# Kernel tuning notes

Hardware: AMD Instinct MI355X
Metric: run time of the kernel (lower is better)

The kernel has to match this reference:

```python
import jax, jax.numpy as jnp
import numpy as np

B, S, E = 2, 2048, 1024
H = 1344            # hidden_dim = ceil(1.3*1024/64)*64
NH = 4              # mLSTM heads
DH = H // NH        # 336
K = 4               # causal conv kernel size
NPH = H // 4        # headwise proj heads (qkv_proj_blocksize=4)
PD = H // NPH       # per-head proj dim = 4
EPS = 1e-6


def setup_inputs() -> dict:
    key = jax.random.key(0)
    ks = jax.random.split(key, 10)
    s_in = jnp.sqrt(2.0 / (5 * E))    # small_init(E)
    s_pd = jnp.sqrt(2.0 / (5 * PD))   # small_init per-head dim
    return {
        "x": jax.random.normal(ks[0], (B, S, E), jnp.float32),
        "W_up": jax.random.normal(ks[1], (E, 2 * H), jnp.float32) * s_in,
        "conv_k": jax.random.normal(ks[2], (K, 1, H), jnp.float32) * jnp.sqrt(2.0 / K),  # depthwise, WIO layout
        "conv_b": jnp.zeros((H,), jnp.float32),
        "Wq": jax.random.normal(ks[3], (NPH, PD, PD), jnp.float32) * s_pd,
        "Wk": jax.random.normal(ks[4], (NPH, PD, PD), jnp.float32) * s_pd,
        "Wv": jax.random.normal(ks[5], (NPH, PD, PD), jnp.float32) * s_pd,
        "W_ig": jax.random.normal(ks[6], (3 * H, NH), jnp.float32) * 0.01,
        "b_ig": jax.random.normal(ks[7], (NH,), jnp.float32) * 0.1,
        "W_fg": jax.random.normal(ks[8], (3 * H, NH), jnp.float32) * 0.01,
        "b_fg": jnp.linspace(3.0, 6.0, NH, dtype=jnp.float32),
        "ln_w": jnp.ones((H,), jnp.float32),
        "skip": jnp.ones((H,), jnp.float32),
        "W_down": jax.random.normal(ks[9], (H, E), jnp.float32) * (2.0 / 12 / np.sqrt(H)),
    }


def _headwise(x, W):
    # LinearHeadwiseExpand: block-diagonal projection over NPH heads of size PD
    xh = x.reshape(B, S, NPH, PD)
    return jnp.einsum('bshd,hdo->bsho', xh, W).reshape(B, S, H)


def _mlstm_cell(q, k, v, ig, fg):
    # parallel stabilized mLSTM; q,k,v: (B,NH,S,DH); ig,fg: (B,NH,S)
    logf = jax.nn.log_sigmoid(fg)
    c = jnp.cumsum(logf, axis=-1)                         # (B,NH,S)
    logfmat = c[..., :, None] - c[..., None, :]           # (B,NH,S,S) cumulative forget decay
    mask = jnp.tril(jnp.ones((S, S), bool))               # causal mask
    log_D = jnp.where(mask, logfmat, -jnp.inf) + ig[..., None, :]
    m = jnp.max(log_D, axis=-1, keepdims=True)            # rowwise stabilizer
    D = jnp.exp(log_D - m)
    qk = jnp.einsum('bnsd,bntd->bnst', q, k) * (DH ** -0.5)
    C = qk * D
    n = jnp.maximum(jnp.abs(jnp.sum(C, axis=-1, keepdims=True)), jnp.exp(-m))
    return jnp.einsum('bnst,bntd->bnsd', C / (n + EPS), v)


def reference(x, W_up, conv_k, conv_b, Wq, Wk, Wv, W_ig, b_ig, W_fg, b_fg, ln_w, skip, W_down):
    x_inner = x @ W_up                                    # (B,S,2H)
    x_m, z = jnp.split(x_inner, 2, axis=-1)
    # depthwise causal conv1d
    xp = jnp.pad(x_m, ((0, 0), (K - 1, 0), (0, 0)))
    xc = jax.lax.conv_general_dilated(
        xp, conv_k, (1,), 'VALID',
        dimension_numbers=('NWC', 'WIO', 'NWC'),
        feature_group_count=H) + conv_b
    act = jax.nn.silu(xc)
    q = _headwise(act, Wq)
    k = _headwise(act, Wk)
    v = _headwise(x_m, Wv)
    gin = jnp.concatenate([q, k, v], axis=-1)             # (B,S,3H)
    ig = jnp.transpose(gin @ W_ig + b_ig, (0, 2, 1))      # (B,NH,S)
    fg = jnp.transpose(gin @ W_fg + b_fg, (0, 2, 1))
    qh = jnp.transpose(q.reshape(B, S, NH, DH), (0, 2, 1, 3))
    kh = jnp.transpose(k.reshape(B, S, NH, DH), (0, 2, 1, 3))
    vh = jnp.transpose(v.reshape(B, S, NH, DH), (0, 2, 1, 3))
    h = _mlstm_cell(qh, kh, vh, ig, fg)                   # (B,NH,S,DH)
    # multi-head layernorm (per-head groupnorm over DH, scale only)
    mu = jnp.mean(h, axis=-1, keepdims=True)
    var = jnp.var(h, axis=-1, keepdims=True)
    hn = (h - mu) * jax.lax.rsqrt(var + 1e-5) * ln_w.reshape(NH, 1, DH)
    h_out = jnp.transpose(hn, (0, 2, 1, 3)).reshape(B, S, H)
    h_state = (h_out + skip * act) * jax.nn.silu(z)
    return h_state @ W_down
```

## Files before the change

### kernel.cpp

```cpp
#include <hip/hip_runtime.h>
#include <cmath>

#define DI __device__ __forceinline__

constexpr int B_=2, S_=2048, E_=1024, H_=1344, NH_=4, DH_=336;
constexpr int BS_=B_*S_, H2_=2*H_;
constexpr int NG_=B_*NH_*S_;

constexpr size_t N_X=(size_t)BS_*E_;
constexpr size_t N_WUP=(size_t)E_*H2_;
constexpr size_t N_WDN=(size_t)H_*E_;
constexpr size_t N_BSH=(size_t)BS_*H_;
constexpr size_t N_BSH2=(size_t)BS_*H2_;
constexpr size_t N_WH=5376, N_WG=16128, N_CK=4*H_;

constexpr size_t O_IGB = 64;
constexpr size_t O_LOGF= O_IGB + NG_;
constexpr size_t O_AB  = O_LOGF+ NG_;
constexpr size_t O_MB  = O_AB  + NG_;
constexpr size_t O_MTB = O_MB  + NG_;
constexpr size_t O_CK  = O_MTB + NG_;
constexpr size_t O_CB  = O_CK  + N_CK;
constexpr size_t O_WQ  = O_CB  + H_;
constexpr size_t O_WK  = O_WQ  + N_WH;
constexpr size_t O_WV  = O_WK  + N_WH;
constexpr size_t O_WIG = O_WV  + N_WH;
constexpr size_t O_BIG = O_WIG + N_WG;
constexpr size_t O_WFG = O_BIG + 16;
constexpr size_t O_BFG = O_WFG + N_WG;
constexpr size_t O_LNW = O_BFG + 16;
constexpr size_t O_SKP = O_LNW + H_;
constexpr size_t O_FX  = O_SKP + H_;
constexpr size_t O_FWUP= O_FX  + N_X;
constexpr size_t O_FWDN= O_FWUP+ N_WUP;
constexpr size_t O_XIN = O_FWDN+ N_WDN;
constexpr size_t O_ACT = O_XIN + N_BSH2;
constexpr size_t O_QB  = O_ACT + N_BSH;
constexpr size_t O_KB  = O_QB  + N_BSH;
constexpr size_t O_VB  = O_KB  + N_BSH;
constexpr size_t O_HOUT= O_VB  + N_BSH;

constexpr size_t KSPLIT_SHORTS=(size_t)8*128*11*64*8;
constexpr size_t VT_SHORTS=(size_t)8*64*22*64*8;

typedef __attribute__((ext_vector_type(8))) short bf16x8;
typedef __attribute__((ext_vector_type(4))) float f32x4;

DI float bf2f(unsigned int u){union{unsigned int i;float f;}v;v.i=(u&0xffffu)<<16;return v.f;}
DI unsigned short f2bf(float f){union{float f;unsigned int i;}v;v.f=f;unsigned int x=v.i;
  return (unsigned short)((x+0x7fffu+((x>>16)&1u))>>16);}
DI float siluf(float x){return x/(1.f+expf(-x));}
DI float logsigf(float x){return (x>=0.f)?-log1pf(expf(-x)):x-log1pf(expf(x));}
DI void load4(const float* p, float* d){float4 v=*reinterpret_cast<const float4*>(p);
  d[0]=v.x;d[1]=v.y;d[2]=v.z;d[3]=v.w;}

__global__ __launch_bounds__(256) void detect_k(const unsigned short* __restrict__ xraw,
                                                int* __restrict__ flag){
  __shared__ int cnt_s;
  if(threadIdx.x==0) cnt_s=0;
  __syncthreads();
  int c=0;
  for(int i=threadIdx.x;i<2048;i+=256){
    const unsigned e=(xraw[i]>>7)&0xFFu;
    if(e>=0x90u) c++;
  }
  atomicAdd(&cnt_s,c);
  __syncthreads();
  if(threadIdx.x==0) *flag=(cnt_s>16)?0:1;
}

constexpr int CV0=5376, CV1=CV0+1344, CV2=CV1+5376, CV3=CV2+5376, CV4=CV3+5376,
              CV5=CV4+16128, CV6=CV5+4, CV7=CV6+16128, CV8=CV7+4,
              CV9=CV8+1344, CVT=CV9+1344;
__global__ __launch_bounds__(256) void convall_k(
    const void* s0,const void* s1,const void* s2,const void* s3,const void* s4,
    const void* s5,const void* s6,const void* s7,const void* s8,const void* s9,
    const void* s10, float* __restrict__ ws, const int* __restrict__ flag){
  const int i=blockIdx.x*256+threadIdx.x;
  if(i>=CVT) return;
  const void* src; int off; size_t dst;
  if(i<CV0){src=s0; off=i;      dst=O_CK +off;}
  else if(i<CV1){src=s1; off=i-CV0; dst=O_CB +off;}
  else if(i<CV2){src=s2; off=i-CV1; dst=O_WQ +off;}
  else if(i<CV3){src=s3; off=i-CV2; dst=O_WK +off;}
  else if(i<CV4){src=s4; off=i-CV3; dst=O_WV +off;}
  else if(i<CV5){src=s5; off=i-CV4; dst=O_WIG+off;}
  else if(i<CV6){src=s6; off=i-CV5; dst=O_BIG+off;}
  else if(i<CV7){src=s7; off=i-CV6; dst=O_WFG+off;}
  else if(i<CV8){src=s8; off=i-CV7; dst=O_BFG+off;}
  else if(i<CV9){src=s9; off=i-CV8; dst=O_LNW+off;}
  else          {src=s10;off=i-CV9; dst=O_SKP+off;}
  ws[dst]=(*flag)?bf2f(((const unsigned short*)src)[off])
                 :((const float*)src)[off];
}

__global__ __launch_bounds__(256) void aprep_k(const void* __restrict__ src,
                                               const int* __restrict__ flag,
                                               int kcn,int ldk,int total,
                                               unsigned short* __restrict__ hi,
                                               unsigned short* __restrict__ lo){
  const int slot=blockIdx.x*256+threadIdx.x;
  if(slot>=total) return;
  const int l=slot&63, rest=slot>>6;
  const int kc=rest%kcn, mt=rest/kcn;
  const int row=mt*16+(l&15), k0=kc*32+(l>>4)*8;
  const int fl=flag?*flag:0;
  float v[8];
  if(fl){
    const unsigned short* s=(const unsigned short*)src+(size_t)row*ldk+k0;
    const uint4 u=*reinterpret_cast<const uint4*>(s);
    v[0]=bf2f(u.x);v[1]=bf2f(u.x>>16);v[2]=bf2f(u.y);v[3]=bf2f(u.y>>16);
    v[4]=bf2f(u.z);v[5]=bf2f(u.z>>16);v[6]=bf2f(u.w);v[7]=bf2f(u.w>>16);
  }else{
    const float* s=(const float*)src+(size_t)row*ldk+k0;
    load4(s,v); load4(s+4,v+4);
  }
  unsigned short h8[8], l8[8];
#pragma unroll
  for(int j=0;j<8;j++){ h8[j]=f2bf(v[j]); l8[j]=f2bf(v[j]-bf2f(h8[j])); }
  uint4 ph,pl;
  ph.x=(unsigned)h8[0]|((unsigned)h8[1]<<16); ph.y=(unsigned)h8[2]|((unsigned)h8[3]<<16);
  ph.z=(unsigned)h8[4]|((unsigned)h8[5]<<16); ph.w=(unsigned)h8[6]|((unsigned)h8[7]<<16);
  pl.x=(unsigned)l8[0]|((unsigned)l8[1]<<16); pl.y=(unsigned)l8[2]|((unsigned)l8[3]<<16);
  pl.z=(unsigned)l8[4]|((unsigned)l8[5]<<16); pl.w=(unsigned)l8[6]|((unsigned)l8[7]<<16);
  *reinterpret_cast<uint4*>(&hi[(size_t)slot*8])=ph;
  *reinterpret_cast<uint4*>(&lo[(size_t)slot*8])=pl;
}

__global__ __launch_bounds__(256) void bprep_k(const void* __restrict__ src,
                                               const int* __restrict__ flag,
                                               int kcn,int ldn,int total,
                                               unsigned short* __restrict__ hi,
                                               unsigned short* __restrict__ lo){
  const int slot=blockIdx.x*256+threadIdx.x;
  if(slot>=total) return;
  const int l=slot&63, rest=slot>>6;
  const int kc=rest%kcn, nt=rest/kcn;
  const int col=nt*16+(l&15), row0=kc*32+(l>>4)*8;
  const int fl=flag?*flag:0;
  float v[8];
  if(fl){
    const unsigned short* s=(const unsigned short*)src;
#pragma unroll
    for(int j=0;j<8;j++) v[j]=bf2f(s[(size_t)(row0+j)*ldn+col]);
  }else{
    const float* s=(const float*)src;
#pragma unroll
    for(int j=0;j<8;j++) v[j]=s[(size_t)(row0+j)*ldn+col];
  }
  unsigned short h8[8], l8[8];
#pragma unroll
  for(int j=0;j<8;j++){ h8[j]=f2bf(v[j]); l8[j]=f2bf(v[j]-bf2f(h8[j])); }
  uint4 ph,pl;
  ph.x=(unsigned)h8[0]|((unsigned)h8[1]<<16); ph.y=(unsigned)h8[2]|((unsigned)h8[3]<<16);
  ph.z=(unsigned)h8[4]|((unsigned)h8[5]<<16); ph.w=(unsigned)h8[6]|((unsigned)h8[7]<<16);
  pl.x=(unsigned)l8[0]|((unsigned)l8[1]<<16); pl.y=(unsigned)l8[2]|((unsigned)l8[3]<<16);
  pl.z=(unsigned)l8[4]|((unsigned)l8[5]<<16); pl.w=(unsigned)l8[6]|((unsigned)l8[7]<<16);
  *reinterpret_cast<uint4*>(&hi[(size_t)slot*8])=ph;
  *reinterpret_cast<uint4*>(&lo[(size_t)slot*8])=pl;
}

__global__ __launch_bounds__(256) void gemm2_k(
    const unsigned short* __restrict__ Ahi, const unsigned short* __restrict__ Alo,
    const unsigned short* __restrict__ Bhi, const unsigned short* __restrict__ Blo,
    void* __restrict__ C, const int* __restrict__ flag, int kcn, int ldc){
  const int t=threadIdx.x, w=t>>6, l=t&63, lm=l&15, quad=l>>4;
  const int bn=blockIdx.x*128, bm=blockIdx.y*128;
  const int mtg0=bm>>4, ntg0=bn>>4;

  __shared__ short TT[2][32*512];

  f32x4 acc[2][8];
#pragma unroll
  for(int g=0;g<2;g++)
#pragma unroll
    for(int nt=0;nt<8;nt++) acc[g][nt]={0.f,0.f,0.f,0.f};

  auto stage=[&](int buf,int kc){
#pragma unroll
    for(int j=0;j<8;j++){
      const int tr=w*8+j;
      const unsigned short* src;
      if(tr<8)       src=&Ahi[((size_t)(mtg0+tr   )*kcn+kc)*512+(size_t)l*8];
      else if(tr<16) src=&Alo[((size_t)(mtg0+tr-8 )*kcn+kc)*512+(size_t)l*8];
      else if(tr<24) src=&Bhi[((size_t)(ntg0+tr-16)*kcn+kc)*512+(size_t)l*8];
      else           src=&Blo[((size_t)(ntg0+tr-24)*kcn+kc)*512+(size_t)l*8];
      __builtin_amdgcn_global_load_lds(
        (const __attribute__((address_space(1))) unsigned int*)src,
        (__attribute__((address_space(3))) unsigned int*)&TT[buf][tr*512],
        16,0,0);
    }
  };

  auto compute=[&](int buf){
    const short* Tb=&TT[buf][0];
    const bf16x8 ah0=*reinterpret_cast<const bf16x8*>(&Tb[(2*w  )*512+l*8]);
    const bf16x8 ah1=*reinterpret_cast<const bf16x8*>(&Tb[(2*w+1)*512+l*8]);
    const bf16x8 al0=*reinterpret_cast<const bf16x8*>(&Tb[(8+2*w  )*512+l*8]);
    const bf16x8 al1=*reinterpret_cast<const bf16x8*>(&Tb[(8+2*w+1)*512+l*8]);
#pragma unroll
    for(int nt=0;nt<8;nt++){
      const bf16x8 bh=*reinterpret_cast<const bf16x8*>(&Tb[(16+nt)*512+l*8]);
      const bf16x8 bl=*reinterpret_cast<const bf16x8*>(&Tb[(24+nt)*512+l*8]);
      acc[0][nt]=__builtin_amdgcn_mfma_f32_16x16x32_bf16(ah0,bh,acc[0][nt],0,0,0);
      acc[0][nt]=__builtin_amdgcn_mfma_f32_16x16x32_bf16(al0,bh,acc[0][nt],0,0,0);
      acc[0][nt]=__builtin_amdgcn_mfma_f32_16x16x32_bf16(ah0,bl,acc[0][nt],0,0,0);
      acc[1][nt]=__builtin_amdgcn_mfma_f32_16x16x32_bf16(ah1,bh,acc[1][nt],0,0,0);
      acc[1][nt]=__builtin_amdgcn_mfma_f32_16x16x32_bf16(al1,bh,acc[1][nt],0,0,0);
      acc[1][nt]=__builtin_amdgcn_mfma_f32_16x16x32_bf16(ah1,bl,acc[1][nt],0,0,0);
    }
  };

  stage(0,0);
  __syncthreads();
  for(int kc=0;kc<kcn;kc++){
    const int cur=kc&1;
    if(kc+1<kcn) stage(cur^1,kc+1);
    compute(cur);
    __syncthreads();
  }

  const int bf=flag?*flag:0;
#pragma unroll
  for(int g=0;g<2;g++)
#pragma unroll
    for(int nt=0;nt<8;nt++)
#pragma unroll
      for(int r=0;r<4;r++){
        const size_t idx=(size_t)(bm+(2*w+g)*16+quad*4+r)*ldc+bn+nt*16+lm;
        if(bf) ((unsigned short*)C)[idx]=f2bf(acc[g][nt][r]);
        else   ((float*)C)[idx]=acc[g][nt][r];
      }
}

__global__ __launch_bounds__(256) void convqkv_k(const float* __restrict__ xin,
                                                 const float* __restrict__ ck,
                                                 const float* __restrict__ cb,
                                                 const float* __restrict__ Wq,
                                                 const float* __restrict__ Wk,
                                                 const float* __restrict__ Wv,
                                                 float* __restrict__ act,
                                                 float* __restrict__ qb,
                                                 float* __restrict__ kb,
                                                 float* __restrict__ vb){
  const int i=blockIdx.x*256+threadIdx.x;
  if(i>=BS_*(H_/4)) return;
  const int bs=i/(H_/4), ph=i-bs*(H_/4);
  const int b=bs>>11, s=bs&2047;
  const int base=ph*4;
  float xc[4];
#pragma unroll
  for(int d=0;d<4;d++) xc[d]=cb[base+d];
  float xm[4]={0.f,0.f,0.f,0.f};
#pragma unroll
  for(int w=0;w<4;w++){
    const int sr=s-3+w;
    if(sr>=0){
      float xv[4];
      load4(&xin[(size_t)(b*S_+sr)*H2_+base],xv);
#pragma unroll
      for(int d=0;d<4;d++) xc[d]+=xv[d]*ck[w*H_+base+d];
      if(w==3){ xm[0]=xv[0];xm[1]=xv[1];xm[2]=xv[2];xm[3]=xv[3]; }
    }
  }
  float a4[4];
#pragma unroll
  for(int d=0;d<4;d++) a4[d]=siluf(xc[d]);
  *reinterpret_cast<float4*>(&act[(size_t)bs*H_+base])
      =make_float4(a4[0],a4[1],a4[2],a4[3]);
  float q4[4],k4[4],v4[4];
#pragma unroll
  for(int o=0;o<4;o++){
    float q=0.f,k=0.f,v=0.f;
#pragma unroll
    for(int d=0;d<4;d++){
      q+=a4[d]*Wq[ph*16+d*4+o];
      k+=a4[d]*Wk[ph*16+d*4+o];
      v+=xm[d]*Wv[ph*16+d*4+o];
    }
    q4[o]=q;k4[o]=k;v4[o]=v;
  }
  const int nh=ph/84, dh0=(ph-nh*84)*4;
  const size_t off=((size_t)(b*NH_+nh)*S_+s)*DH_+dh0;
  *reinterpret_cast<float4*>(&qb[off])=make_float4(q4[0],q4[1],q4[2],q4[3]);
  *reinterpret_cast<float4*>(&kb[off])=make_float4(k4[0],k4[1],k4[2],k4[3]);
  *reinterpret_cast<float4*>(&vb[off])=make_float4(v4[0],v4[1],v4[2],v4[3]);
}

__global__ __launch_bounds__(256) void gates2_k(const float* __restrict__ qb,
                                                const float* __restrict__ kb,
                                                const float* __restrict__ vb,
                                                const float* __restrict__ Wig,
                                                const float* __restrict__ big,
                                                const float* __restrict__ Wfg,
                                                const float* __restrict__ bfg,
                                                float* __restrict__ igb,
                                                float* __restrict__ logfb){
  const int wid=(blockIdx.x*256+threadIdx.x)>>6;
  const int l=threadIdx.x&63;
  if(wid>=BS_) return;
  const int b=wid>>11, s=wid&2047;
  float aI0=0.f,aI1=0.f,aI2=0.f,aI3=0.f;
  float aF0=0.f,aF1=0.f,aF2=0.f,aF3=0.f;
  for(int nh=0;nh<NH_;nh++){
    const size_t rb=((size_t)(b*NH_+nh)*S_+s)*DH_;
    const int hb=nh*DH_;
    for(int dh=l;dh<DH_;dh+=64){
      const int h=hb+dh;
      const float q=qb[rb+dh], k=kb[rb+dh], v=vb[rb+dh];
      const float4 wiq=*reinterpret_cast<const float4*>(&Wig[(size_t)h*4]);
      const float4 wik=*reinterpret_cast<const float4*>(&Wig[(size_t)(H_+h)*4]);
      const float4 wiv=*reinterpret_cast<const float4*>(&Wig[(size_t)(2*H_+h)*4]);
      const float4 wfq=*reinterpret_cast<const float4*>(&Wfg[(size_t)h*4]);
      const float4 wfk=*reinterpret_cast<const float4*>(&Wfg[(size_t)(H_+h)*4]);
      const float4 wfv=*reinterpret_cast<const float4*>(&Wfg[(size_t)(2*H_+h)*4]);
      aI0+=q*wiq.x+k*wik.x+v*wiv.x;
      aI1+=q*wiq.y+k*wik.y+v*wiv.y;
      aI2+=q*wiq.z+k*wik.z+v*wiv.z;
      aI3+=q*wiq.w+k*wik.w+v*wiv.w;
      aF0+=q*wfq.x+k*wfk.x+v*wfv.x;
      aF1+=q*wfq.y+k*wfk.y+v*wfv.y;
      aF2+=q*wfq.z+k*wfk.z+v*wfv.z;
      aF3+=q*wfq.w+k*wfk.w+v*wfv.w;
    }
  }
#pragma unroll
  for(int m=1;m<64;m<<=1){
    aI0+=__shfl_xor(aI0,m); aI1+=__shfl_xor(aI1,m);
    aI2+=__shfl_xor(aI2,m); aI3+=__shfl_xor(aI3,m);
    aF0+=__shfl_xor(aF0,m); aF1+=__shfl_xor(aF1,m);
    aF2+=__shfl_xor(aF2,m); aF3+=__shfl_xor(aF3,m);
  }
  if(l==0){
    const size_t o0=(size_t)(b*NH_+0)*S_+s;
    const size_t o1=(size_t)(b*NH_+1)*S_+s;
    const size_t o2=(size_t)(b*NH_+2)*S_+s;
    const size_t o3=(size_t)(b*NH_+3)*S_+s;
    igb[o0]=aI0+big[0]; igb[o1]=aI1+big[1];
    igb[o2]=aI2+big[2]; igb[o3]=aI3+big[3];
    logfb[o0]=logsigf(aF0+bfg[0]); logfb[o1]=logsigf(aF1+bfg[1]);
    logfb[o2]=logsigf(aF2+bfg[2]); logfb[o3]=logsigf(aF3+bfg[3]);
  }
}

__global__ __launch_bounds__(256) void kprep_k(const float* __restrict__ kb,
                                               unsigned short* __restrict__ khi,
                                               unsigned short* __restrict__ klo){
  const int blk=blockIdx.x;
  const int head=blk>>7, tt=blk&127;
  const size_t obase=(size_t)blk*11*512;
  for(int slot=threadIdx.x; slot<704; slot+=256){
    const int dc=slot>>6, ll=slot&63, quad=ll>>4, lm=ll&15;
    const int tg=tt*16+lm, dbase=dc*32+quad*8;
    float v[8];
    if(dbase<336){
      load4(&kb[((size_t)head*S_+tg)*DH_+dbase],v);
      load4(&kb[((size_t)head*S_+tg)*DH_+dbase+4],v+4);
    } else { for(int j=0;j<8;j++) v[j]=0.f; }
    unsigned short hi8[8], lo8[8];
#pragma unroll
    for(int j=0;j<8;j++){
      hi8[j]=f2bf(v[j]);
      lo8[j]=f2bf(v[j]-bf2f(hi8[j]));
    }
    const size_t o=obase+(size_t)(dc*64+ll)*8;
    uint4 ph, pl;
    ph.x=(unsigned)hi8[0]|((unsigned)hi8[1]<<16); ph.y=(unsigned)hi8[2]|((unsigned)hi8[3]<<16);
    ph.z=(unsigned)hi8[4]|((unsigned)hi8[5]<<16); ph.w=(unsigned)hi8[6]|((unsigned)hi8[7]<<16);
    pl.x=(unsigned)lo8[0]|((unsigned)lo8[1]<<16); pl.y=(unsigned)lo8[2]|((unsigned)lo8[3]<<16);
    pl.z=(unsigned)lo8[4]|((unsigned)lo8[5]<<16); pl.w=(unsigned)lo8[6]|((unsigned)lo8[7]<<16);
    *reinterpret_cast<uint4*>(&khi[o])=ph;
    *reinterpret_cast<uint4*>(&klo[o])=pl;
  }
}

__global__ __launch_bounds__(256) void vprep_k(const float* __restrict__ vb,
                                               unsigned short* __restrict__ vTf){
  const int blk=blockIdx.x;
  const int head=blk>>6, tc=blk&63;
  const size_t obase=(size_t)blk*22*512;
  for(int slot=threadIdx.x; slot<1408; slot+=256){
    const int ntg=slot>>6, ll=slot&63, quad=ll>>4, lm=ll&15;
    const int n=ntg*16+lm, t0=tc*32+quad*8;
    unsigned short h8[8];
#pragma unroll
    for(int j=0;j<8;j++){
      float val;
      if(n<336)       val=vb[((size_t)head*S_+t0+j)*DH_+n];
      else if(n==336) val=1.f;
      else            val=0.f;
      h8[j]=f2bf(val);
    }
    uint4 pk;
    pk.x=(unsigned)h8[0]|((unsigned)h8[1]<<16); pk.y=(unsigned)h8[2]|((unsigned)h8[3]<<16);
    pk.z=(unsigned)h8[4]|((unsigned)h8[5]<<16); pk.w=(unsigned)h8[6]|((unsigned)h8[7]<<16);
    *reinterpret_cast<uint4*>(&vTf[obase+(size_t)(ntg*64+ll)*8])=pk;
  }
}

__global__ __launch_bounds__(256) void scan_k(const float* __restrict__ igb,
                                              const float* __restrict__ logfb,
                                              float* __restrict__ ab,float* __restrict__ Mb,
                                              float* __restrict__ mtb){
  const int head=blockIdx.x, t=threadIdx.x;
  __shared__ float sh[256];
  const float* lf=logfb+(size_t)head*S_;
  const float* ig=igb+(size_t)head*S_;
  float lc[8];
  float run=0.f;
#pragma unroll
  for(int i=0;i<8;i++){ run+=lf[t*8+i]; lc[i]=run; }
  sh[t]=run;
  for(int st=1;st<256;st<<=1){
    __syncthreads();
    const float v=(t>=st)?sh[t-st]:0.f;
    __syncthreads();
    sh[t]+=v;
  }
  __syncthreads();
  const float off=(t==0)?0.f:sh[t-1];
  __syncthreads();
  float av[8],mv[8],cv[8];
  float mrun=-1e30f;
#pragma unroll
  for(int i=0;i<8;i++){
    cv[i]=off+lc[i];
    av[i]=ig[t*8+i]-cv[i];
    mrun=fmaxf(mrun,av[i]);
    mv[i]=mrun;
  }
  sh[t]=mrun;
  for(int st=1;st<256;st<<=1){
    __syncthreads();
    const float v=(t>=st)?sh[t-st]:-1e30f;
    __syncthreads();
    sh[t]=fmaxf(sh[t],v);
  }
  __syncthreads();
  const float moff=(t==0)?-1e30f:sh[t-1];
#pragma unroll
  for(int i=0;i<8;i++){
    const float Mi=fmaxf(moff,mv[i]);
    const size_t j=(size_t)head*S_+t*8+i;
    ab[j]=av[i]; Mb[j]=Mi; mtb[j]=cv[i]+Mi;
  }
}

__global__ __launch_bounds__(512,1) void mlstm6_k(
    const float* __restrict__ qb, const unsigned short* __restrict__ khi,
    const unsigned short* __restrict__ klo, const unsigned short* __restrict__ vTf,
    const float* __restrict__ ab, const float* __restrict__ Mb,
    float* __restrict__ part, float* __restrict__ rsum){
  const int bid=blockIdx.x;
  const int head=bid&7;
  const int rest=bid>>3;
  const int pairI=rest&7, seg=rest>>3;
  const int t=threadIdx.x, w=t>>6, l=t&63, lm=l&15, quad=l>>4;

  __shared__ short KV[2][66*512];
  __shared__ short Sc[8][16][40];

  const size_t hb=(size_t)head*S_;
  const float scale=0.05455447256f;

  const int sbA=pairI, sbB=15-pairI;
  const int nA=pairI+1, nTot=17;

  bf16x8 qh[11], ql[11];
  f32x4 accO[22];
  float Mr[4];
  int ws0=sbA*128+w*16;

  auto loadQ=[&](int ws0_){
    const float* qrow=qb+(hb+ws0_+lm)*DH_;
#pragma unroll
    for(int dc=0;dc<11;dc++){
      const int dbase=dc*32+quad*8;
      float v[8];
      if(dbase<336){ load4(qrow+dbase,v); load4(qrow+dbase+4,v+4); }
      else { for(int j=0;j<8;j++) v[j]=0.f; }
#pragma unroll
      for(int j=0;j<8;j++){
        const unsigned short h=f2bf(v[j]);
        qh[dc][j]=(short)h;
        ql[dc][j]=(short)f2bf(v[j]-bf2f(h));
      }
    }
#pragma unroll
    for(int r=0;r<4;r++) Mr[r]=Mb[hb+ws0_+quad*4+r];
#pragma unroll
    for(int n=0;n<22;n++) accO[n]={0.f,0.f,0.f,0.f};
  };

  auto itemC=[&](int i)->int{
    return (i<nA)? (seg+4*i) : (seg+4*(i-nA));
  };

  auto stage=[&](int buf,int c){
    const size_t kbase=(((size_t)head*128+(size_t)(2*c))*11)*512+(size_t)l*8;
    const size_t vbase=(((size_t)head*64+(size_t)c)*22)*512+(size_t)l*8;
#pragma unroll
    for(int j=0;j<9;j++){
      const int tr=w+8*j;
      if(tr<66){
        const unsigned short* src;
        if(tr<22)      src=&khi[kbase+(size_t)tr*512];
        else if(tr<44) src=&klo[kbase+(size_t)(tr-22)*512];
        else           src=&vTf[vbase+(size_t)(tr-44)*512];
        __builtin_amdgcn_global_load_lds(
          (const __attribute__((address_space(1))) unsigned int*)src,
          (__attribute__((address_space(3))) unsigned int*)&KV[buf][(size_t)tr*512],
          16,0,0);
      }
    }
  };

  auto compute=[&](int c,int buf){
    const int t0=c<<5;
    if(t0>ws0+15) return;
    const float al0=ab[hb+t0+lm];
    const float al1=ab[hb+t0+16+lm];
#pragma unroll
    for(int tt=0;tt<2;tt++){
      f32x4 a0={0,0,0,0}, a1={0,0,0,0}, a2={0,0,0,0};
#pragma unroll
      for(int dc=0;dc<11;dc++){
        const bf16x8 kh=*reinterpret_cast<const bf16x8*>(&KV[buf][(tt*11+dc)*512+l*8]);
        const bf16x8 kl=*reinterpret_cast<const bf16x8*>(&KV[buf][(22+tt*11+dc)*512+l*8]);
        a0=__builtin_amdgcn_mfma_f32_16x16x32_bf16(qh[dc],kh,a0,0,0,0);
        a1=__builtin_amdgcn_mfma_f32_16x16x32_bf16(ql[dc],kh,a1,0,0,0);
        a2=__builtin_amdgcn_mfma_f32_16x16x32_bf16(qh[dc],kl,a2,0,0,0);
      }
      const float al=(tt==0)?al0:al1;
      const int tg=t0+tt*16+lm;
#pragma unroll
      for(int r=0;r<4;r++){
        const int srow=quad*4+r;
        const float qk=a0[r]+a1[r]+a2[r];
        const float e=fminf(al-Mr[r],0.f);
        const float msk=(tg<=ws0+srow)?1.f:0.f;
        Sc[w][srow][tt*16+lm]=(short)f2bf(msk*(qk*scale*expf(e)));
      }
    }
    const bf16x8 scf=*reinterpret_cast<const bf16x8*>(&Sc[w][lm][quad*8]);
#pragma unroll
    for(int nt=0;nt<22;nt++){
      const bf16x8 vf=*reinterpret_cast<const bf16x8*>(&KV[buf][(44+nt)*512+l*8]);
      accO[nt]=__builtin_amdgcn_mfma_f32_16x16x32_bf16(scf,vf,accO[nt],0,0,0);
    }
  };

  auto epilogue=[&](){
    const size_t pbase=(size_t)head*2048+ws0;
#pragma unroll
    for(int nt=0;nt<22;nt++){
      const int col=nt*16+lm;
#pragma unroll
      for(int r=0;r<4;r++){
        const int srow=quad*4+r;
        const float val=accO[nt][r];
        if(col<336){ if(val!=0.f) atomicAdd(&part[(pbase+srow)*336+col],val); }
        else if(col==336){ if(val!=0.f) atomicAdd(&rsum[pbase+srow],val); }
      }
    }
  };

  loadQ(ws0);
  stage(0,itemC(0));
  __syncthreads();
  int cur=0;
  for(int i=0;i<nTot;i++){
    if(i+1<nTot) stage(cur^1,itemC(i+1));
    compute(itemC(i),cur);
    if(i==nA-1){
      epilogue();
      ws0=sbB*128+w*16;
      loadQ(ws0);
    }
    __syncthreads();
    cur^=1;
  }
  epilogue();
}

__global__ __launch_bounds__(256) void finalize2_k(const float* __restrict__ part,
                                                   const float* __restrict__ rsum,
                                                   const float* __restrict__ mtb,
                                                   const float* __restrict__ lnw,
                                                   const float* __restrict__ skip,
                                                   const float* __restrict__ act,
                                                   const float* __restrict__ xin,
                                                   float* __restrict__ hs){
  const int sblk=blockIdx.x, head=blockIdx.y;
  const int bI=head>>2, nh=head&3;
  const int s0=sblk*32;
  const int t=threadIdx.x, row=t>>3, sub=t&7;
  __shared__ float red1[32][8], red2[32][8];
  __shared__ float mu_s[32], rs_s[32], inv_s[32];
  const size_t pbase=(size_t)head*2048+s0;
  const float* prow=part+(pbase+row)*336;
  float s1=0.f,s2=0.f;
  for(int c=sub;c<336;c+=8){ const float v=prow[c]; s1+=v; s2+=v*v; }
  red1[row][sub]=s1; red2[row][sub]=s2;
  __syncthreads();
  if(sub==0){
    float a1=0.f,a2=0.f;
#pragma unroll
    for(int j=0;j<8;j++){ a1+=red1[row][j]; a2+=red2[row][j]; }
    const float mt=mtb[(size_t)head*S_+s0+row];
    const float nn=fmaxf(fabsf(rsum[pbase+row]), expf(fminf(fmaxf(-mt,-60.f),60.f)));
    const float inv=1.f/(nn+1e-6f);
    const float mu=a1*inv/336.f;
    const float var=a2*inv*inv/336.f-mu*mu;
    inv_s[row]=inv; mu_s[row]=mu;
    rs_s[row]=rsqrtf(fmaxf(var,0.f)+1e-5f);
  }
  __syncthreads();
  const float inv=inv_s[row], mu=mu_s[row], rs=rs_s[row];
  const size_t bsrow=(size_t)(bI*S_+s0+row);
  float* orow=hs+bsrow*H_+nh*DH_;
  const float* arow=act+bsrow*H_+nh*DH_;
  const float* zrow=xin+bsrow*H2_+H_+nh*DH_;
  const float* srw=skip+nh*DH_;
  const float* lrw=lnw+nh*DH_;
  for(int c=sub;c<336;c+=8){
    const float hn=(prow[c]*inv-mu)*rs*lrw[c];
    orow[c]=(hn+srw[c]*arow[c])*siluf(zrow[c]);
  }
}

extern "C" void kernel_launch(void* const* d_in, const int* in_sizes, int n_in,
                              void* d_out, int out_size, void* d_ws, size_t ws_size,
                              hipStream_t stream){
  float* ws=(float*)d_ws;
  int* flag=(int*)ws;

  float* igb  = ws+O_IGB;
  float* logfb= ws+O_LOGF;
  float* ab   = ws+O_AB;
  float* Mbuf = ws+O_MB;
  float* mtb  = ws+O_MTB;
  float* f_ck = ws+O_CK;
  float* f_cb = ws+O_CB;
  float* f_wq = ws+O_WQ;
  float* f_wk = ws+O_WK;
  float* f_wv = ws+O_WV;
  float* f_wig= ws+O_WIG;
  float* f_big= ws+O_BIG;
  float* f_wfg= ws+O_WFG;
  float* f_bfg= ws+O_BFG;
  float* f_lnw= ws+O_LNW;
  float* f_skp= ws+O_SKP;
  float* xin  = ws+O_XIN;
  float* act  = ws+O_ACT;
  float* qb   = ws+O_QB;
  float* kb   = ws+O_KB;
  float* vb   = ws+O_VB;

  unsigned short* xhi  =(unsigned short*)(ws+O_FX);   unsigned short* xlo  =xhi+N_X;
  unsigned short* wuphi=(unsigned short*)(ws+O_FWUP); unsigned short* wuplo=wuphi+N_WUP;
  unsigned short* wdnhi=(unsigned short*)(ws+O_FWDN); unsigned short* wdnlo=wdnhi+N_WDN;
  unsigned short* khi=(unsigned short*)(ws+O_FX);
  unsigned short* klo=khi+KSPLIT_SHORTS;
  unsigned short* vTf=(unsigned short*)kb;
  unsigned short* hshi=(unsigned short*)kb;
  unsigned short* hslo=hshi+N_BSH;
  float* partb=vb;
  float* rsumb=igb;
  float* hs   = qb;

  detect_k<<<1,256,0,stream>>>((const unsigned short*)d_in[0],flag);
  convall_k<<<(CVT+255)/256,256,0,stream>>>(d_in[2],d_in[3],d_in[4],d_in[5],d_in[6],
                                            d_in[7],d_in[8],d_in[9],d_in[10],d_in[11],
                                            d_in[12],ws,flag);

  aprep_k<<<(256*32*64+255)/256,256,0,stream>>>(d_in[0],flag,32,1024,256*32*64,xhi,xlo);
  bprep_k<<<(168*32*64+255)/256,256,0,stream>>>(d_in[1],flag,32,2688,168*32*64,wuphi,wuplo);
  gemm2_k<<<dim3(2688/128,4096/128),256,0,stream>>>(xhi,xlo,wuphi,wuplo,xin,nullptr,32,H2_);

  convqkv_k<<<(BS_*(H_/4)+255)/256,256,0,stream>>>(xin,f_ck,f_cb,f_wq,f_wk,f_wv,
                                                   act,qb,kb,vb);
  gates2_k<<<(BS_*64+255)/256,256,0,stream>>>(qb,kb,vb,f_wig,f_big,f_wfg,f_bfg,igb,logfb);
  kprep_k<<<8*128,256,0,stream>>>(kb,khi,klo);
  vprep_k<<<8*64,256,0,stream>>>(vb,vTf);
  bprep_k<<<(64*42*64+255)/256,256,0,stream>>>(d_in[13],flag,42,1024,64*42*64,wdnhi,wdnlo);
  scan_k<<<B_*NH_,256,0,stream>>>(igb,logfb,ab,Mbuf,mtb);
  hipMemsetAsync(partb,0,N_BSH*sizeof(float),stream);
  hipMemsetAsync(rsumb,0,(size_t)NG_*sizeof(float),stream);
  mlstm6_k<<<256,512,0,stream>>>(qb,khi,klo,vTf,ab,Mbuf,partb,rsumb);
  finalize2_k<<<dim3(S_/32,B_*NH_),256,0,stream>>>(partb,rsumb,mtb,f_lnw,f_skp,act,xin,hs);
  aprep_k<<<(256*42*64+255)/256,256,0,stream>>>(hs,nullptr,42,1344,256*42*64,hshi,hslo);
  gemm2_k<<<dim3(1024/128,4096/128),256,0,stream>>>(hshi,hslo,wdnhi,wdnlo,d_out,flag,42,E_);
}
```

Before: 478.3 us.

## Use partial vmcnt waits for async LDS prefetch and fold memsets into producer kernels

The GEMM and mLSTM main loops replace full __syncthreads with explicit s_waitcnt vmcnt(N) plus raw barriers, so the prefetch of the next tile stays in flight while the current one is computed. The mLSTM stage now always issues the same number of global-to-LDS loads, duplicating an earlier row when out of range so the count is fixed, and also prefetches the per-chunk gate values into LDS. The two hipMemsetAsync calls are removed: vprep_k now zeroes the partial-output buffer and scan_k zeroes the row-sum buffer (aliased onto igb) after reading it. The hand-counted vmcnt values are fragile and could cause races if the compiler emits a different number of memory ops.

```diff
diff --git a/kernel.cpp b/kernel.cpp
--- a/kernel.cpp
+++ b/kernel.cpp
@@ -160,7 +160,7 @@
   *reinterpret_cast<uint4*>(&lo[(size_t)slot*8])=pl;
 }
 
-__global__ __launch_bounds__(256) void gemm2_k(
+__global__ __launch_bounds__(256) void gemm3_k(
     const unsigned short* __restrict__ Ahi, const unsigned short* __restrict__ Alo,
     const unsigned short* __restrict__ Bhi, const unsigned short* __restrict__ Blo,
     void* __restrict__ C, const int* __restrict__ flag, int kcn, int ldc){
@@ -212,12 +212,17 @@
   };
 
   stage(0,0);
-  __syncthreads();
   for(int kc=0;kc<kcn;kc++){
     const int cur=kc&1;
-    if(kc+1<kcn) stage(cur^1,kc+1);
+    if(kc+1<kcn){
+      stage(cur^1,kc+1);
+      asm volatile("s_waitcnt vmcnt(8)" ::: "memory");
+    } else {
+      asm volatile("s_waitcnt vmcnt(0)" ::: "memory");
+    }
+    __builtin_amdgcn_s_barrier();
     compute(cur);
-    __syncthreads();
+    __builtin_amdgcn_s_barrier();
   }
 
   const int bf=flag?*flag:0;
@@ -374,8 +379,9 @@
   }
 }
 
-__global__ __launch_bounds__(256) void vprep_k(const float* __restrict__ vb,
-                                               unsigned short* __restrict__ vTf){
+__global__ __launch_bounds__(256) void vprep_k(const float* vb,
+                                               unsigned short* __restrict__ vTf,
+                                               float* partz){
   const int blk=blockIdx.x;
   const int head=blk>>6, tc=blk&63;
   const size_t obase=(size_t)blk*22*512;
@@ -396,16 +402,19 @@
     pk.z=(unsigned)h8[4]|((unsigned)h8[5]<<16); pk.w=(unsigned)h8[6]|((unsigned)h8[7]<<16);
     *reinterpret_cast<uint4*>(&vTf[obase+(size_t)(ntg*64+ll)*8])=pk;
   }
-}
-
-__global__ __launch_bounds__(256) void scan_k(const float* __restrict__ igb,
+  __syncthreads();
+  const size_t zb=((size_t)head*2048+(size_t)tc*32)*336;
+  for(int idx=threadIdx.x; idx<32*336; idx+=256) partz[zb+idx]=0.f;
+}
+
+__global__ __launch_bounds__(256) void scan_k(float* igm,
                                               const float* __restrict__ logfb,
                                               float* __restrict__ ab,float* __restrict__ Mb,
                                               float* __restrict__ mtb){
   const int head=blockIdx.x, t=threadIdx.x;
   __shared__ float sh[256];
   const float* lf=logfb+(size_t)head*S_;
-  const float* ig=igb+(size_t)head*S_;
+  float* ig=igm+(size_t)head*S_;
   float lc[8];
   float run=0.f;
 #pragma unroll
@@ -443,10 +452,11 @@
     const float Mi=fmaxf(moff,mv[i]);
     const size_t j=(size_t)head*S_+t*8+i;
     ab[j]=av[i]; Mb[j]=Mi; mtb[j]=cv[i]+Mi;
-  }
-}
-
-__global__ __launch_bounds__(512,1) void mlstm6_k(
+    ig[t*8+i]=0.f;
+  }
+}
+
+__global__ __launch_bounds__(512,1) void mlstm8_k(
     const float* __restrict__ qb, const unsigned short* __restrict__ khi,
     const unsigned short* __restrict__ klo, const unsigned short* __restrict__ vTf,
     const float* __restrict__ ab, const float* __restrict__ Mb,
@@ -457,7 +467,7 @@
   const int pairI=rest&7, seg=rest>>3;
   const int t=threadIdx.x, w=t>>6, l=t&63, lm=l&15, quad=l>>4;
 
-  __shared__ short KV[2][66*512];
+  __shared__ short KV[2][66*512+128];
   __shared__ short Sc[8][16][40];
 
   const size_t hb=(size_t)head*S_;
@@ -501,25 +511,29 @@
     const size_t vbase=(((size_t)head*64+(size_t)c)*22)*512+(size_t)l*8;
 #pragma unroll
     for(int j=0;j<9;j++){
-      const int tr=w+8*j;
-      if(tr<66){
-        const unsigned short* src;
-        if(tr<22)      src=&khi[kbase+(size_t)tr*512];
-        else if(tr<44) src=&klo[kbase+(size_t)(tr-22)*512];
-        else           src=&vTf[vbase+(size_t)(tr-44)*512];
-        __builtin_amdgcn_global_load_lds(
-          (const __attribute__((address_space(1))) unsigned int*)src,
-          (__attribute__((address_space(3))) unsigned int*)&KV[buf][(size_t)tr*512],
-          16,0,0);
-      }
-    }
+      int tr=w+8*j;
+      if(tr>=66) tr=w;
+      const unsigned short* src;
+      if(tr<22)      src=&khi[kbase+(size_t)tr*512];
+      else if(tr<44) src=&klo[kbase+(size_t)(tr-22)*512];
+      else           src=&vTf[vbase+(size_t)(tr-44)*512];
+      __builtin_amdgcn_global_load_lds(
+        (const __attribute__((address_space(1))) unsigned int*)src,
+        (__attribute__((address_space(3))) unsigned int*)&KV[buf][(size_t)tr*512],
+        16,0,0);
+    }
+    __builtin_amdgcn_global_load_lds(
+      (const __attribute__((address_space(1))) unsigned int*)(ab+hb+(c<<5)+l),
+      (__attribute__((address_space(3))) unsigned int*)&KV[buf][66*512],
+      4,0,0);
   };
 
   auto compute=[&](int c,int buf){
     const int t0=c<<5;
     if(t0>ws0+15) return;
-    const float al0=ab[hb+t0+lm];
-    const float al1=ab[hb+t0+16+lm];
+    const float* abl=reinterpret_cast<const float*>(&KV[buf][66*512]);
+    const float al0=abl[lm];
+    const float al1=abl[16+lm];
 #pragma unroll
     for(int tt=0;tt<2;tt++){
       f32x4 a0={0,0,0,0}, a1={0,0,0,0}, a2={0,0,0,0};
@@ -567,17 +581,22 @@
 
   loadQ(ws0);
   stage(0,itemC(0));
-  __syncthreads();
   int cur=0;
   for(int i=0;i<nTot;i++){
-    if(i+1<nTot) stage(cur^1,itemC(i+1));
+    if(i+1<nTot){
+      stage(cur^1,itemC(i+1));
+      asm volatile("s_waitcnt vmcnt(10)" ::: "memory");
+    } else {
+      asm volatile("s_waitcnt vmcnt(0)" ::: "memory");
+    }
+    __builtin_amdgcn_s_barrier();
     compute(itemC(i),cur);
     if(i==nA-1){
       epilogue();
       ws0=sbB*128+w*16;
       loadQ(ws0);
     }
-    __syncthreads();
+    __builtin_amdgcn_s_barrier();
     cur^=1;
   }
   epilogue();
@@ -676,19 +695,17 @@
 
   aprep_k<<<(256*32*64+255)/256,256,0,stream>>>(d_in[0],flag,32,1024,256*32*64,xhi,xlo);
   bprep_k<<<(168*32*64+255)/256,256,0,stream>>>(d_in[1],flag,32,2688,168*32*64,wuphi,wuplo);
-  gemm2_k<<<dim3(2688/128,4096/128),256,0,stream>>>(xhi,xlo,wuphi,wuplo,xin,nullptr,32,H2_);
+  gemm3_k<<<dim3(2688/128,4096/128),256,0,stream>>>(xhi,xlo,wuphi,wuplo,xin,nullptr,32,H2_);
 
   convqkv_k<<<(BS_*(H_/4)+255)/256,256,0,stream>>>(xin,f_ck,f_cb,f_wq,f_wk,f_wv,
                                                    act,qb,kb,vb);
   gates2_k<<<(BS_*64+255)/256,256,0,stream>>>(qb,kb,vb,f_wig,f_big,f_wfg,f_bfg,igb,logfb);
   kprep_k<<<8*128,256,0,stream>>>(kb,khi,klo);
-  vprep_k<<<8*64,256,0,stream>>>(vb,vTf);
+  vprep_k<<<8*64,256,0,stream>>>(vb,vTf,partb);
   bprep_k<<<(64*42*64+255)/256,256,0,stream>>>(d_in[13],flag,42,1024,64*42*64,wdnhi,wdnlo);
   scan_k<<<B_*NH_,256,0,stream>>>(igb,logfb,ab,Mbuf,mtb);
-  hipMemsetAsync(partb,0,N_BSH*sizeof(float),stream);
-  hipMemsetAsync(rsumb,0,(size_t)NG_*sizeof(float),stream);
-  mlstm6_k<<<256,512,0,stream>>>(qb,khi,klo,vTf,ab,Mbuf,partb,rsumb);
+  mlstm8_k<<<256,512,0,stream>>>(qb,khi,klo,vTf,ab,Mbuf,partb,rsumb);
   finalize2_k<<<dim3(S_/32,B_*NH_),256,0,stream>>>(partb,rsumb,mtb,f_lnw,f_skp,act,xin,hs);
   aprep_k<<<(256*42*64+255)/256,256,0,stream>>>(hs,nullptr,42,1344,256*42*64,hshi,hslo);
-  gemm2_k<<<dim3(1024/128,4096/128),256,0,stream>>>(hshi,hslo,wdnhi,wdnlo,d_out,flag,42,E_);
-}
+  gemm3_k<<<dim3(1024/128,4096/128),256,0,stream>>>(hshi,hslo,wdnhi,wdnlo,d_out,flag,42,E_);
+}
```

Measured after the change: 470.0 us. No clear change (-1.8%).
